# Kernel optimization log

Hardware: AMD Instinct MI355X
Metric: run time of the kernel (lower is better)

## Reference

```python
import jax, jax.numpy as jnp
import numpy as np


def setup_inputs() -> dict:
    key = jax.random.key(0)
    ks = jax.random.split(key, 12)
    T, B, D, H = 512, 256, 256, 512
    s = 0.02  # small init scale for numerical stability of the recurrence
    return {
        "inputs": jax.random.normal(ks[0], (T, B, D), jnp.float32),
        "lstm_Wih": jax.random.normal(ks[1], (4 * H, D + H), jnp.float32) * s,
        "lstm_Whh": jax.random.normal(ks[2], (4 * H, H), jnp.float32) * s,
        "lstm_bih": jax.random.normal(ks[3], (4 * H,), jnp.float32) * s,
        "lstm_bhh": jax.random.normal(ks[4], (4 * H,), jnp.float32) * s,
        "phase": jax.random.normal(ks[5], (H, H), jnp.float32) * s,
        "fe_W": jax.random.normal(ks[6], (H, H), jnp.float32) * s,
        "fe_b": jax.random.normal(ks[7], (H,), jnp.float32) * s,
        "gru_Wih": jax.random.normal(ks[8], (3 * H, H), jnp.float32) * s,
        "gru_Whh": jax.random.normal(ks[9], (3 * H, H), jnp.float32) * s,
        "gru_bih": jax.random.normal(ks[10], (3 * H,), jnp.float32) * s,
        "gru_bhh": jax.random.normal(ks[11], (3 * H,), jnp.float32) * s,
    }


def reference(inputs, lstm_Wih, lstm_Whh, lstm_bih, lstm_bhh, phase,
              fe_W, fe_b, gru_Wih, gru_Whh, gru_bih, gru_bhh):
    T, B, D = inputs.shape
    H = lstm_Whh.shape[1]

    def step(carry, x):
        hx, cx = carry  # [B, H] each
        combined = jnp.concatenate([x, hx], axis=1)  # [B, D+H]
        # LSTMCell (PyTorch gate order: i, f, g, o)
        gates = combined @ lstm_Wih.T + lstm_bih + hx @ lstm_Whh.T + lstm_bhh
        i, f, g, o = jnp.split(gates, 4, axis=1)
        i = jax.nn.sigmoid(i)
        f = jax.nn.sigmoid(f)
        g = jnp.tanh(g)
        o = jax.nn.sigmoid(o)
        cx_new = f * cx + i * g
        hx_new = o * jnp.tanh(cx_new)
        # phase-shift matmul
        hx_new = hx_new @ phase
        # feature extractor linear
        hx_new = hx_new @ fe_W.T + fe_b
        # GRUCell with input = hidden = hx_new (PyTorch gate order: r, z, n)
        gi = hx_new @ gru_Wih.T + gru_bih
        gh = hx_new @ gru_Whh.T + gru_bhh
        ir, iz, inn = jnp.split(gi, 3, axis=1)
        hr, hz, hn = jnp.split(gh, 3, axis=1)
        r = jax.nn.sigmoid(ir + hr)
        z = jax.nn.sigmoid(iz + hz)
        n = jnp.tanh(inn + r * hn)
        hx_new = (1.0 - z) * n + z * hx_new
        return (hx_new, cx_new), hx_new

    hx0 = jnp.zeros((B, H), inputs.dtype)
    cx0 = jnp.zeros((B, H), inputs.dtype)
    (hx, cx), outputs = jax.lax.scan(step, (hx0, cx0), inputs)
    return outputs, hx, cx
```

## Files before the change

### kernel.cpp

```cpp
#include <hip/hip_runtime.h>


#define T_ 512
#define B_ 256
#define D_ 256
#define H_ 512

typedef short v8s __attribute__((ext_vector_type(8)));
typedef float v4f __attribute__((ext_vector_type(4)));

__device__ __forceinline__ unsigned short f2bf(float f) {
  unsigned u = __float_as_uint(f);
  u = u + 0x7FFFu + ((u >> 16) & 1u);
  return (unsigned short)(u >> 16);
}

__device__ __forceinline__ float sigf(float x) {
  return 1.0f / (1.0f + __expf(-x));
}


__global__ __launch_bounds__(256) void k_setup_w1(
    const float* __restrict__ Wih, const float* __restrict__ Whh,
    const float* __restrict__ bih, const float* __restrict__ bhh,
    unsigned short* __restrict__ W1, float* __restrict__ b1)
{
  int idx = blockIdx.x * 256 + threadIdx.x;
  if (idx < 2048 * 768) {
    int n = idx / 768;
    int k = idx - n * 768;
    float v = Wih[idx];
    if (k >= 256) v += Whh[n * 512 + (k - 256)];
    W1[idx] = f2bf(v);
  }
  if (idx < 2048) b1[idx] = bih[idx] + bhh[idx];
}

__global__ __launch_bounds__(256) void k_m1(
    const float* __restrict__ phase, const float* __restrict__ feW,
    float* __restrict__ M1f)
{
  int idx = blockIdx.x * 256 + threadIdx.x;
  int k = idx >> 9, n = idx & 511;
  const float* pr = phase + k * 512;
  const float* fr = feW + n * 512;
  float s = 0.f;
  #pragma unroll 8
  for (int j = 0; j < 512; ++j) s += pr[j] * fr[j];
  M1f[idx] = s;
}

__global__ __launch_bounds__(256) void k_setup_w2(
    const float* __restrict__ M1f, const float* __restrict__ gWih,
    const float* __restrict__ gWhh, unsigned short* __restrict__ W2)
{
  int idx = blockIdx.x * 256 + threadIdx.x;
  if (idx >= 2560 * 512) return;
  int np = idx >> 9;
  int k  = idx & 511;
  const float* m1k = M1f + k * 512;
  float s = 0.f;
  if (np < 512) {
    s = m1k[np];
  } else if (np < 1536) {
    int c = np - 512;
    const float* a = gWih + c * 512;
    const float* b = gWhh + c * 512;
    #pragma unroll 8
    for (int n = 0; n < 512; ++n) s += m1k[n] * (a[n] + b[n]);
  } else if (np < 2048) {
    int c = np - 1536 + 1024;
    const float* a = gWih + c * 512;
    #pragma unroll 8
    for (int n = 0; n < 512; ++n) s += m1k[n] * a[n];
  } else {
    int c = np - 2048 + 1024;
    const float* b = gWhh + c * 512;
    #pragma unroll 8
    for (int n = 0; n < 512; ++n) s += m1k[n] * b[n];
  }
  W2[idx] = f2bf(s);
}

__global__ __launch_bounds__(256) void k_setup_bias2(
    const float* __restrict__ feb, const float* __restrict__ gWih,
    const float* __restrict__ gWhh, const float* __restrict__ gbih,
    const float* __restrict__ gbhh, float* __restrict__ bias2)
{
  int np = blockIdx.x * 256 + threadIdx.x;
  if (np >= 2560) return;
  float s;
  if (np < 512) {
    s = feb[np];
  } else if (np < 1536) {
    int c = np - 512;
    s = gbih[c] + gbhh[c];
    for (int n = 0; n < 512; ++n) s += feb[n] * (gWih[c * 512 + n] + gWhh[c * 512 + n]);
  } else if (np < 2048) {
    int c = np - 1536 + 1024;
    s = gbih[c];
    for (int n = 0; n < 512; ++n) s += feb[n] * gWih[c * 512 + n];
  } else {
    int c = np - 2048 + 1024;
    s = gbhh[c];
    for (int n = 0; n < 512; ++n) s += feb[n] * gWhh[c * 512 + n];
  }
  bias2[np] = s;
}

__global__ __launch_bounds__(256) void k_init(
    unsigned short* __restrict__ hx, float* __restrict__ cx)
{
  int i = blockIdx.x * 256 + threadIdx.x;
  if (i < B_ * H_) { hx[i] = 0; cx[i] = 0.f; }
}


__global__ __launch_bounds__(256) void k_stage1(
    const float* __restrict__ xt,
    const unsigned short* __restrict__ hx,
    const unsigned short* __restrict__ W1,
    const float* __restrict__ b1,
    float* __restrict__ cx,
    unsigned short* __restrict__ h1)
{
  __shared__ float lds[4][32][17];
  int blk = blockIdx.x;
  int mt = blk >> 5, jt = blk & 31;
  int m0 = mt << 5, j0 = jt << 4;
  int tid = threadIdx.x;
  int w = tid >> 6;
  int lane = tid & 63;
  int l15 = lane & 15;
  int quad = lane >> 4;

  v4f acc0 = {0.f, 0.f, 0.f, 0.f}, acc1 = {0.f, 0.f, 0.f, 0.f};
  const unsigned short* Bp = W1 + (size_t)((w << 9) + j0 + l15) * 768 + (quad << 3);
  const float* xp0 = xt + (m0 + l15) * 256 + (quad << 3);
  const unsigned short* hp0 = hx + (m0 + l15) * 512 + (quad << 3);

  #pragma unroll 4
  for (int kc = 0; kc < 24; ++kc) {
    v8s bfrag = *(const v8s*)(Bp + kc * 32);
    v8s a0, a1;
    if (kc < 8) {
      const float* p0 = xp0 + kc * 32;
      const float* p1 = p0 + 16 * 256;
      #pragma unroll
      for (int i = 0; i < 8; ++i) {
        a0[i] = (short)f2bf(p0[i]);
        a1[i] = (short)f2bf(p1[i]);
      }
    } else {
      const unsigned short* q0 = hp0 + (kc - 8) * 32;
      a0 = *(const v8s*)q0;
      a1 = *(const v8s*)(q0 + 16 * 512);
    }
    acc0 = __builtin_amdgcn_mfma_f32_16x16x32_bf16(a0, bfrag, acc0, 0, 0, 0);
    acc1 = __builtin_amdgcn_mfma_f32_16x16x32_bf16(a1, bfrag, acc1, 0, 0, 0);
  }
  #pragma unroll
  for (int r = 0; r < 4; ++r) {
    int m = (quad << 2) + r;
    lds[w][m][l15] = acc0[r];
    lds[w][m + 16][l15] = acc1[r];
  }
  __syncthreads();
  #pragma unroll
  for (int p = tid; p < 512; p += 256) {
    int m = p >> 4, j = p & 15;
    int jg = j0 + j;
    int b = m0 + m;
    float iv = sigf(lds[0][m][j] + b1[jg]);
    float fv = sigf(lds[1][m][j] + b1[512 + jg]);
    float gv = tanhf(lds[2][m][j] + b1[1024 + jg]);
    float ov = sigf(lds[3][m][j] + b1[1536 + jg]);
    int o = b * 512 + jg;
    float c = fv * cx[o] + iv * gv;
    cx[o] = c;
    h1[o] = f2bf(ov * tanhf(c));
  }
}

__global__ __launch_bounds__(256) void k_stage2(
    const unsigned short* __restrict__ h1,
    const unsigned short* __restrict__ W2,
    const float* __restrict__ bias2,
    unsigned short* __restrict__ hx,
    float* __restrict__ out_t)
{
  __shared__ float lds[5][32][17];
  int blk = blockIdx.x;
  int mt = blk >> 5, jt = blk & 31;
  int m0 = mt << 5, j0 = jt << 4;
  int tid = threadIdx.x;
  int w = tid >> 6, lane = tid & 63, l15 = lane & 15, quad = lane >> 4;
  int mh = w & 1;
  int ga = w >> 1;
  int gb = ga + 2;

  const unsigned short* Ap = h1 + (size_t)(m0 + (mh << 4) + l15) * 512 + (quad << 3);
  const unsigned short* Ba = W2 + (size_t)((ga << 9) + j0 + l15) * 512 + (quad << 3);
  const unsigned short* Bb = W2 + (size_t)((gb << 9) + j0 + l15) * 512 + (quad << 3);
  const unsigned short* Bc = W2 + (size_t)((4  << 9) + j0 + l15) * 512 + (quad << 3);

  v4f acca = {0.f,0.f,0.f,0.f}, accb = {0.f,0.f,0.f,0.f}, accc = {0.f,0.f,0.f,0.f};
  #pragma unroll 4
  for (int kc = 0; kc < 16; ++kc) {
    v8s a = *(const v8s*)(Ap + kc * 32);
    acca = __builtin_amdgcn_mfma_f32_16x16x32_bf16(a, *(const v8s*)(Ba + kc * 32), acca, 0, 0, 0);
    accb = __builtin_amdgcn_mfma_f32_16x16x32_bf16(a, *(const v8s*)(Bb + kc * 32), accb, 0, 0, 0);
    accc = __builtin_amdgcn_mfma_f32_16x16x32_bf16(a, *(const v8s*)(Bc + kc * 32), accc, 0, 0, 0);
  }
  int mbase = (mh << 4) + (quad << 2);
  #pragma unroll
  for (int r = 0; r < 4; ++r) {
    lds[ga][mbase + r][l15] = acca[r];
    lds[gb][mbase + r][l15] = accb[r];
  }
  if (w < 2) {
    #pragma unroll
    for (int r = 0; r < 4; ++r) lds[4][mbase + r][l15] = accc[r];
  }
  __syncthreads();
  #pragma unroll
  for (int p = tid; p < 512; p += 256) {
    int m = p >> 4, j = p & 15;
    int jg = j0 + j, b = m0 + m;
    float h3 = lds[0][m][j] + bias2[jg];
    float rv = sigf(lds[1][m][j] + bias2[512 + jg]);
    float zv = sigf(lds[2][m][j] + bias2[1024 + jg]);
    float nv = tanhf(lds[3][m][j] + bias2[1536 + jg] + rv * (lds[4][m][j] + bias2[2048 + jg]));
    float hnew = (1.f - zv) * nv + zv * h3;
    int o = b * 512 + jg;
    hx[o] = f2bf(hnew);
    out_t[o] = hnew;
  }
}

__global__ __launch_bounds__(256) void k_final(
    float* __restrict__ out, const float* __restrict__ cx)
{
  int i = blockIdx.x * 256 + threadIdx.x;
  if (i < B_ * H_) {
    out[67108864 + i] = out[66977792 + i];
    out[67108864 + 131072 + i] = cx[i];
  }
}


extern "C" void kernel_launch(void* const* d_in, const int* in_sizes, int n_in,
                              void* d_out, int out_size, void* d_ws, size_t ws_size,
                              hipStream_t stream)
{
  const float* x     = (const float*)d_in[0];
  const float* Wih   = (const float*)d_in[1];
  const float* Whh   = (const float*)d_in[2];
  const float* bih   = (const float*)d_in[3];
  const float* bhh   = (const float*)d_in[4];
  const float* phase = (const float*)d_in[5];
  const float* feW   = (const float*)d_in[6];
  const float* feb   = (const float*)d_in[7];
  const float* gWih  = (const float*)d_in[8];
  const float* gWhh  = (const float*)d_in[9];
  const float* gbih  = (const float*)d_in[10];
  const float* gbhh  = (const float*)d_in[11];

  char* p = (char*)d_ws;
  unsigned short* W1 = (unsigned short*)p; p += (size_t)2048 * 768 * 2;
  unsigned short* W2 = (unsigned short*)p; p += (size_t)2560 * 512 * 2;
  float* b1    = (float*)p; p += 2048 * 4;
  float* bias2 = (float*)p; p += 2560 * 4;
  float* M1f   = (float*)p; p += (size_t)512 * 512 * 4;
  unsigned short* hx = (unsigned short*)p; p += (size_t)B_ * H_ * 2;
  unsigned short* h1 = (unsigned short*)p; p += (size_t)B_ * H_ * 2;
  float* cx    = (float*)p; p += (size_t)B_ * H_ * 4;

  k_setup_w1<<<6144, 256, 0, stream>>>(Wih, Whh, bih, bhh, W1, b1);
  k_m1<<<1024, 256, 0, stream>>>(phase, feW, M1f);
  k_setup_w2<<<5120, 256, 0, stream>>>(M1f, gWih, gWhh, W2);
  k_setup_bias2<<<10, 256, 0, stream>>>(feb, gWih, gWhh, gbih, gbhh, bias2);
  k_init<<<512, 256, 0, stream>>>(hx, cx);

  float* out = (float*)d_out;
  for (int t = 0; t < T_; ++t) {
    k_stage1<<<256, 256, 0, stream>>>(x + (size_t)t * (B_ * D_), hx, W1, b1, cx, h1);
    k_stage2<<<256, 256, 0, stream>>>(h1, W2, bias2, hx, out + (size_t)t * (B_ * H_));
  }
  k_final<<<512, 256, 0, stream>>>(out, cx);
}
```

Measured before the change: 14.63 ms.

## Fuse recurrent steps into a persistent cooperative kernel with grid barriers

Replaces the 1024 per-timestep kernel launches with one cooperative persistent kernel that loops over all timesteps, using a custom hierarchical atomic grid barrier between the LSTM and GRU stages. W1 fragments are held in registers, each block's W2 slice is cached in swizzled LDS, and the cell state stays in LDS. The next timestep's input is pre-converted to bf16 into a double buffer. This removes launch overhead and repeated weight loads, at the cost of spin-wait barrier latency and a dependence on all 256 blocks being co-resident.

```diff
diff --git a/kernel.cpp b/kernel.cpp
--- a/kernel.cpp
+++ b/kernel.cpp
@@ -109,142 +109,217 @@
 }
 
 __global__ __launch_bounds__(256) void k_init(
-    unsigned short* __restrict__ hx, float* __restrict__ cx)
+    unsigned short* __restrict__ hx, unsigned* __restrict__ bar)
 {
   int i = blockIdx.x * 256 + threadIdx.x;
-  if (i < B_ * H_) { hx[i] = 0; cx[i] = 0.f; }
-}
-
-
-__global__ __launch_bounds__(256) void k_stage1(
-    const float* __restrict__ xt,
-    const unsigned short* __restrict__ hx,
+  ((unsigned*)hx)[i] = 0u;
+  if (i < 2048) bar[i] = 0u;
+}
+
+
+__device__ __forceinline__ void gridbar(unsigned* bar, int grpsel, unsigned k) {
+  asm volatile("" ::: "memory");
+  __syncthreads();
+  if (threadIdx.x == 0) {
+    unsigned old = __hip_atomic_fetch_add(bar + grpsel * 32, 1u,
+                                          __ATOMIC_ACQ_REL, __HIP_MEMORY_SCOPE_AGENT);
+    if (old == k * 8u - 1u)
+      __hip_atomic_fetch_add(bar + 1024, 1u,
+                             __ATOMIC_ACQ_REL, __HIP_MEMORY_SCOPE_AGENT);
+    while (__hip_atomic_load(bar + 1024, __ATOMIC_RELAXED,
+                             __HIP_MEMORY_SCOPE_AGENT) < k * 32u) {}
+    (void)__hip_atomic_load(bar + 1024, __ATOMIC_ACQUIRE, __HIP_MEMORY_SCOPE_AGENT);
+  }
+  __syncthreads();
+  asm volatile("" ::: "memory");
+}
+
+
+__global__ __launch_bounds__(256, 1) void k_persist(
+    const float* __restrict__ x,
     const unsigned short* __restrict__ W1,
     const float* __restrict__ b1,
-    float* __restrict__ cx,
-    unsigned short* __restrict__ h1)
-{
-  __shared__ float lds[4][32][17];
-  int blk = blockIdx.x;
-  int mt = blk >> 5, jt = blk & 31;
-  int m0 = mt << 5, j0 = jt << 4;
-  int tid = threadIdx.x;
-  int w = tid >> 6;
-  int lane = tid & 63;
-  int l15 = lane & 15;
-  int quad = lane >> 4;
-
-  v4f acc0 = {0.f, 0.f, 0.f, 0.f}, acc1 = {0.f, 0.f, 0.f, 0.f};
-  const unsigned short* Bp = W1 + (size_t)((w << 9) + j0 + l15) * 768 + (quad << 3);
-  const float* xp0 = xt + (m0 + l15) * 256 + (quad << 3);
-  const unsigned short* hp0 = hx + (m0 + l15) * 512 + (quad << 3);
-
-  #pragma unroll 4
-  for (int kc = 0; kc < 24; ++kc) {
-    v8s bfrag = *(const v8s*)(Bp + kc * 32);
-    v8s a0, a1;
-    if (kc < 8) {
-      const float* p0 = xp0 + kc * 32;
-      const float* p1 = p0 + 16 * 256;
-      #pragma unroll
-      for (int i = 0; i < 8; ++i) {
-        a0[i] = (short)f2bf(p0[i]);
-        a1[i] = (short)f2bf(p1[i]);
-      }
-    } else {
-      const unsigned short* q0 = hp0 + (kc - 8) * 32;
-      a0 = *(const v8s*)q0;
-      a1 = *(const v8s*)(q0 + 16 * 512);
-    }
-    acc0 = __builtin_amdgcn_mfma_f32_16x16x32_bf16(a0, bfrag, acc0, 0, 0, 0);
-    acc1 = __builtin_amdgcn_mfma_f32_16x16x32_bf16(a1, bfrag, acc1, 0, 0, 0);
-  }
-  #pragma unroll
-  for (int r = 0; r < 4; ++r) {
-    int m = (quad << 2) + r;
-    lds[w][m][l15] = acc0[r];
-    lds[w][m + 16][l15] = acc1[r];
-  }
-  __syncthreads();
-  #pragma unroll
-  for (int p = tid; p < 512; p += 256) {
-    int m = p >> 4, j = p & 15;
-    int jg = j0 + j;
-    int b = m0 + m;
-    float iv = sigf(lds[0][m][j] + b1[jg]);
-    float fv = sigf(lds[1][m][j] + b1[512 + jg]);
-    float gv = tanhf(lds[2][m][j] + b1[1024 + jg]);
-    float ov = sigf(lds[3][m][j] + b1[1536 + jg]);
-    int o = b * 512 + jg;
-    float c = fv * cx[o] + iv * gv;
-    cx[o] = c;
-    h1[o] = f2bf(ov * tanhf(c));
-  }
-}
-
-__global__ __launch_bounds__(256) void k_stage2(
-    const unsigned short* __restrict__ h1,
     const unsigned short* __restrict__ W2,
     const float* __restrict__ bias2,
     unsigned short* __restrict__ hx,
-    float* __restrict__ out_t)
-{
-  __shared__ float lds[5][32][17];
-  int blk = blockIdx.x;
-  int mt = blk >> 5, jt = blk & 31;
-  int m0 = mt << 5, j0 = jt << 4;
-  int tid = threadIdx.x;
-  int w = tid >> 6, lane = tid & 63, l15 = lane & 15, quad = lane >> 4;
-  int mh = w & 1;
-  int ga = w >> 1;
-  int gb = ga + 2;
-
-  const unsigned short* Ap = h1 + (size_t)(m0 + (mh << 4) + l15) * 512 + (quad << 3);
-  const unsigned short* Ba = W2 + (size_t)((ga << 9) + j0 + l15) * 512 + (quad << 3);
-  const unsigned short* Bb = W2 + (size_t)((gb << 9) + j0 + l15) * 512 + (quad << 3);
-  const unsigned short* Bc = W2 + (size_t)((4  << 9) + j0 + l15) * 512 + (quad << 3);
-
-  v4f acca = {0.f,0.f,0.f,0.f}, accb = {0.f,0.f,0.f,0.f}, accc = {0.f,0.f,0.f,0.f};
-  #pragma unroll 4
-  for (int kc = 0; kc < 16; ++kc) {
-    v8s a = *(const v8s*)(Ap + kc * 32);
-    acca = __builtin_amdgcn_mfma_f32_16x16x32_bf16(a, *(const v8s*)(Ba + kc * 32), acca, 0, 0, 0);
-    accb = __builtin_amdgcn_mfma_f32_16x16x32_bf16(a, *(const v8s*)(Bb + kc * 32), accb, 0, 0, 0);
-    accc = __builtin_amdgcn_mfma_f32_16x16x32_bf16(a, *(const v8s*)(Bc + kc * 32), accc, 0, 0, 0);
-  }
-  int mbase = (mh << 4) + (quad << 2);
-  #pragma unroll
-  for (int r = 0; r < 4; ++r) {
-    lds[ga][mbase + r][l15] = acca[r];
-    lds[gb][mbase + r][l15] = accb[r];
-  }
-  if (w < 2) {
+    unsigned short* __restrict__ h1,
+    unsigned short* __restrict__ xb0,
+    unsigned short* __restrict__ xb1,
+    float* __restrict__ out,
+    unsigned* __restrict__ bar)
+{
+  __shared__ __align__(16) char w2s[49152];
+  __shared__ float ew[3136];
+  __shared__ float cxs[512];
+  __shared__ float b1s[64];
+  __shared__ float b2s[48];
+
+  const int tid  = threadIdx.x;
+  const int b    = blockIdx.x;
+  const int w    = tid >> 6;
+  const int lane = tid & 63;
+  const int l15  = lane & 15;
+  const int quad = lane >> 4;
+  const int m0A  = (b >> 5) << 5;
+  const int j0A  = (b & 31) << 4;
+  const int m0B  = (b >> 6) << 6;
+  const int jbB  = b & 63;
+  const int grpsel = b & 31;
+  const unsigned swz = (unsigned)((l15 & 7) << 4);
+
+  for (int u = tid; u < 2560; u += 256) {
+    int r = u >> 6, c = u & 63;
+    int g = r >> 3, jj = r & 7;
+    const unsigned short* src = W2 + (size_t)(g * 512 + (jbB << 3) + jj) * 512 + (c << 3);
+    *(v8s*)(w2s + r * 1024 + (((unsigned)(c << 4)) ^ ((unsigned)((r & 7) << 4)))) =
+        *(const v8s*)src;
+  }
+  {
+    v8s z = {0, 0, 0, 0, 0, 0, 0, 0};
+    for (int u = tid; u < 512; u += 256) {
+      int r = 40 + (u >> 6), c = u & 63;
+      *(v8s*)(w2s + r * 1024 + (((unsigned)(c << 4)) ^ ((unsigned)((r & 7) << 4)))) = z;
+    }
+  }
+  if (tid < 64) b1s[tid] = b1[((tid >> 4) << 9) + j0A + (tid & 15)];
+  if (tid < 40) b2s[tid] = bias2[((tid >> 3) << 9) + (jbB << 3) + (tid & 7)];
+  for (int u = tid; u < 512; u += 256) cxs[u] = 0.f;
+  {
+    int i = (b << 8) + tid;
+    xb0[i] = f2bf(x[i]);
+  }
+  v8s bw1[24];
+  {
+    const unsigned short* Bp = W1 + (size_t)((w << 9) + j0A + l15) * 768 + (quad << 3);
     #pragma unroll
-    for (int r = 0; r < 4; ++r) lds[4][mbase + r][l15] = accc[r];
-  }
-  __syncthreads();
-  #pragma unroll
-  for (int p = tid; p < 512; p += 256) {
+    for (int kc = 0; kc < 24; ++kc) bw1[kc] = *(const v8s*)(Bp + kc * 32);
+  }
+  const unsigned short* ap_h = hx + ((m0A + l15) << 9) + (quad << 3);
+  const unsigned short* apB  = h1 + ((m0B + (w << 4) + l15) << 9) + (quad << 3);
+
+  gridbar(bar, grpsel, 1u);
+
+  for (int t = 0; t < T_; ++t) {
+    {
+      const unsigned short* ap_x = ((t & 1) ? xb1 : xb0) + ((m0A + l15) << 8) + (quad << 3);
+      v4f a00 = {0.f, 0.f, 0.f, 0.f};
+      v4f a01 = a00, a10 = a00, a11 = a00;
+      #pragma unroll
+      for (int kk = 0; kk < 12; ++kk) {
+        v8s f0, f1;
+        if (kk < 8) {
+          f0 = *(const v8s*)(ap_x + kk * 32);
+          f1 = *(const v8s*)(ap_x + kk * 32 + 4096);
+        } else {
+          f0 = *(const v8s*)(ap_h + (kk - 8) * 32);
+          f1 = *(const v8s*)(ap_h + (kk - 8) * 32 + 8192);
+        }
+        v8s g0 = *(const v8s*)(ap_h + (kk + 4) * 32);
+        v8s g1 = *(const v8s*)(ap_h + (kk + 4) * 32 + 8192);
+        a00 = __builtin_amdgcn_mfma_f32_16x16x32_bf16(f0, bw1[kk],      a00, 0, 0, 0);
+        a10 = __builtin_amdgcn_mfma_f32_16x16x32_bf16(f1, bw1[kk],      a10, 0, 0, 0);
+        a01 = __builtin_amdgcn_mfma_f32_16x16x32_bf16(g0, bw1[12 + kk], a01, 0, 0, 0);
+        a11 = __builtin_amdgcn_mfma_f32_16x16x32_bf16(g1, bw1[12 + kk], a11, 0, 0, 0);
+      }
+      v4f s0 = a00 + a01;
+      v4f s1 = a10 + a11;
+      {
+        float* eb = ew + (w * 32 + (quad << 2)) * 17 + l15;
+        #pragma unroll
+        for (int r = 0; r < 4; ++r) { eb[r * 17] = s0[r]; eb[(r + 16) * 17] = s1[r]; }
+      }
+      __syncthreads();
+      {
+        int p = tid << 1;
+        int m = p >> 4, j = p & 15;
+        const float* e = ew + m * 17 + j;
+        float ia = sigf(e[0]     + b1s[j]);
+        float ib = sigf(e[1]     + b1s[j + 1]);
+        float fa = sigf(e[544]   + b1s[16 + j]);
+        float fb = sigf(e[545]   + b1s[17 + j]);
+        float ga = tanhf(e[1088] + b1s[32 + j]);
+        float gb = tanhf(e[1089] + b1s[33 + j]);
+        float oa = sigf(e[1632]  + b1s[48 + j]);
+        float ob = sigf(e[1633]  + b1s[49 + j]);
+        float ca = fa * cxs[p]     + ia * ga;
+        float cb = fb * cxs[p + 1] + ib * gb;
+        cxs[p] = ca; cxs[p + 1] = cb;
+        unsigned hv = (unsigned)f2bf(oa * tanhf(ca)) |
+                      ((unsigned)f2bf(ob * tanhf(cb)) << 16);
+        *(unsigned*)(h1 + ((size_t)(m0A + m) << 9) + j0A + j) = hv;
+      }
+    }
+    gridbar(bar, grpsel, (unsigned)(2 * t + 2));
+    {
+      if (t < T_ - 1) {
+        unsigned short* xbn = (t & 1) ? xb0 : xb1;
+        int i = (b << 8) + tid;
+        xbn[i] = f2bf(x[((size_t)(t + 1) << 16) + i]);
+      }
+      v4f c00 = {0.f, 0.f, 0.f, 0.f};
+      v4f c01 = c00, c10 = c00, c11 = c00, c20 = c00, c21 = c00;
+      #pragma unroll
+      for (int kk = 0; kk < 8; ++kk) {
+        v8s q0 = *(const v8s*)(apB + kk * 32);
+        v8s q1 = *(const v8s*)(apB + kk * 32 + 256);
+        unsigned oa = (((unsigned)(kk << 6)) | ((unsigned)(quad << 4))) ^ swz;
+        unsigned ob = (((unsigned)((kk + 8) << 6)) | ((unsigned)(quad << 4))) ^ swz;
+        v8s w0a = *(const v8s*)(w2s + (l15)      * 1024 + oa);
+        v8s w1a = *(const v8s*)(w2s + (16 + l15) * 1024 + oa);
+        v8s w2a = *(const v8s*)(w2s + (32 + l15) * 1024 + oa);
+        v8s w0b = *(const v8s*)(w2s + (l15)      * 1024 + ob);
+        v8s w1b = *(const v8s*)(w2s + (16 + l15) * 1024 + ob);
+        v8s w2b = *(const v8s*)(w2s + (32 + l15) * 1024 + ob);
+        c00 = __builtin_amdgcn_mfma_f32_16x16x32_bf16(q0, w0a, c00, 0, 0, 0);
+        c10 = __builtin_amdgcn_mfma_f32_16x16x32_bf16(q0, w1a, c10, 0, 0, 0);
+        c20 = __builtin_amdgcn_mfma_f32_16x16x32_bf16(q0, w2a, c20, 0, 0, 0);
+        c01 = __builtin_amdgcn_mfma_f32_16x16x32_bf16(q1, w0b, c01, 0, 0, 0);
+        c11 = __builtin_amdgcn_mfma_f32_16x16x32_bf16(q1, w1b, c11, 0, 0, 0);
+        c21 = __builtin_amdgcn_mfma_f32_16x16x32_bf16(q1, w2b, c21, 0, 0, 0);
+      }
+      v4f r0 = c00 + c01, r1 = c10 + c11, r2 = c20 + c21;
+      {
+        float* eb = ew + ((w << 4) + (quad << 2)) * 49 + l15;
+        #pragma unroll
+        for (int r = 0; r < 4; ++r) {
+          eb[r * 49]      = r0[r];
+          eb[r * 49 + 16] = r1[r];
+          eb[r * 49 + 32] = r2[r];
+        }
+      }
+      __syncthreads();
+      {
+        int p = tid << 1;
+        int m = p >> 3, jj = p & 7;
+        const float* e = ew + m * 49;
+        float h3a = e[jj]     + b2s[jj];
+        float h3b = e[jj + 1] + b2s[jj + 1];
+        float ra = sigf(e[8 + jj]   + b2s[8 + jj]);
+        float rb = sigf(e[9 + jj]   + b2s[9 + jj]);
+        float za = sigf(e[16 + jj]  + b2s[16 + jj]);
+        float zb = sigf(e[17 + jj]  + b2s[17 + jj]);
+        float na = tanhf(e[24 + jj] + b2s[24 + jj] + ra * (e[32 + jj] + b2s[32 + jj]));
+        float nb = tanhf(e[25 + jj] + b2s[25 + jj] + rb * (e[33 + jj] + b2s[33 + jj]));
+        float ha = (1.f - za) * na + za * h3a;
+        float hb = (1.f - zb) * nb + zb * h3b;
+        size_t o = ((size_t)(m0B + m) << 9) + (jbB << 3) + jj;
+        *(unsigned*)(hx + o) = (unsigned)f2bf(ha) | ((unsigned)f2bf(hb) << 16);
+        float* op = out + ((size_t)t << 17) + o;
+        __builtin_nontemporal_store(ha, op);
+        __builtin_nontemporal_store(hb, op + 1);
+        if (t == T_ - 1) {
+          out[67108864 + o]     = ha;
+          out[67108864 + o + 1] = hb;
+        }
+      }
+    }
+    gridbar(bar, grpsel, (unsigned)(2 * t + 3));
+  }
+  {
+    int p = tid << 1;
     int m = p >> 4, j = p & 15;
-    int jg = j0 + j, b = m0 + m;
-    float h3 = lds[0][m][j] + bias2[jg];
-    float rv = sigf(lds[1][m][j] + bias2[512 + jg]);
-    float zv = sigf(lds[2][m][j] + bias2[1024 + jg]);
-    float nv = tanhf(lds[3][m][j] + bias2[1536 + jg] + rv * (lds[4][m][j] + bias2[2048 + jg]));
-    float hnew = (1.f - zv) * nv + zv * h3;
-    int o = b * 512 + jg;
-    hx[o] = f2bf(hnew);
-    out_t[o] = hnew;
-  }
-}
-
-__global__ __launch_bounds__(256) void k_final(
-    float* __restrict__ out, const float* __restrict__ cx)
-{
-  int i = blockIdx.x * 256 + threadIdx.x;
-  if (i < B_ * H_) {
-    out[67108864 + i] = out[66977792 + i];
-    out[67108864 + 131072 + i] = cx[i];
+    float2 cv; cv.x = cxs[p]; cv.y = cxs[p + 1];
+    *(float2*)(out + 67239936 + ((size_t)(m0A + m) << 9) + j0A + j) = cv;
   }
 }
 
@@ -269,23 +344,35 @@
   char* p = (char*)d_ws;
   unsigned short* W1 = (unsigned short*)p; p += (size_t)2048 * 768 * 2;
   unsigned short* W2 = (unsigned short*)p; p += (size_t)2560 * 512 * 2;
-  float* b1    = (float*)p; p += 2048 * 4;
-  float* bias2 = (float*)p; p += 2560 * 4;
+  float* b1    = (float*)p; p += 8192;
+  float* bias2 = (float*)p; p += 10240;
   float* M1f   = (float*)p; p += (size_t)512 * 512 * 4;
-  unsigned short* hx = (unsigned short*)p; p += (size_t)B_ * H_ * 2;
-  unsigned short* h1 = (unsigned short*)p; p += (size_t)B_ * H_ * 2;
-  float* cx    = (float*)p; p += (size_t)B_ * H_ * 4;
+  unsigned short* hx  = (unsigned short*)p; p += 262144;
+  unsigned short* h1  = (unsigned short*)p; p += 262144;
+  unsigned short* xb0 = (unsigned short*)p; p += 131072;
+  unsigned short* xb1 = (unsigned short*)p; p += 131072;
+  unsigned* bar = (unsigned*)p; p += 8192;
 
   k_setup_w1<<<6144, 256, 0, stream>>>(Wih, Whh, bih, bhh, W1, b1);
   k_m1<<<1024, 256, 0, stream>>>(phase, feW, M1f);
   k_setup_w2<<<5120, 256, 0, stream>>>(M1f, gWih, gWhh, W2);
   k_setup_bias2<<<10, 256, 0, stream>>>(feb, gWih, gWhh, gbih, gbhh, bias2);
-  k_init<<<512, 256, 0, stream>>>(hx, cx);
+  k_init<<<256, 256, 0, stream>>>(hx, bar);
 
   float* out = (float*)d_out;
-  for (int t = 0; t < T_; ++t) {
-    k_stage1<<<256, 256, 0, stream>>>(x + (size_t)t * (B_ * D_), hx, W1, b1, cx, h1);
-    k_stage2<<<256, 256, 0, stream>>>(h1, W2, bias2, hx, out + (size_t)t * (B_ * H_));
-  }
-  k_final<<<512, 256, 0, stream>>>(out, cx);
-}
+  {
+    const float* a0 = x;
+    const unsigned short* a1 = W1;
+    const float* a2 = b1;
+    const unsigned short* a3 = W2;
+    const float* a4 = bias2;
+    unsigned short* a5 = hx;
+    unsigned short* a6 = h1;
+    unsigned short* a7 = xb0;
+    unsigned short* a8 = xb1;
+    float* a9 = out;
+    unsigned* a10 = bar;
+    void* args[11] = {&a0, &a1, &a2, &a3, &a4, &a5, &a6, &a7, &a8, &a9, &a10};
+    hipLaunchCooperativeKernel(k_persist, dim3(256), dim3(256), args, 0u, stream);
+  }
+}
```

Measured after the change: 21.73 ms. +48.5%, slower.
